# Kernel tuning notes

Hardware: AMD Instinct MI355X
Metric: run time of the kernel (lower is better)

The kernel has to match this reference:

```python
import jax, jax.numpy as jnp
import numpy as np

IMAGE_SIZE = (128, 128)
NUM_SLICES = 4
SLICE_SPACING = 0.1
BACKGROUND = 0.0
CHUNK = 1024
N_GAUSS = 4096
EPS = 1e-6


def setup_inputs() -> dict:
    key = jax.random.key(0)
    k1, k2, k3, k4, k5 = jax.random.split(key, 5)
    return {
        "means": jax.random.uniform(k1, (N_GAUSS, 3), dtype=jnp.float32),
        "scales": jax.random.uniform(k2, (N_GAUSS, 3), dtype=jnp.float32),
        "rotations": jax.random.normal(k3, (N_GAUSS, 4), dtype=jnp.float32),
        "opacities": jax.random.uniform(k4, (N_GAUSS, 1), dtype=jnp.float32),
        "features": jax.random.uniform(k5, (N_GAUSS, 1), dtype=jnp.float32),
    }


def _quat_to_rot(q):
    # q: [N,4] (w,x,y,z) -> [N,3,3]
    q = q / jnp.linalg.norm(q, axis=1, keepdims=True)
    w, x, y, z = q[:, 0], q[:, 1], q[:, 2], q[:, 3]
    r0 = jnp.stack([1 - 2 * (y * y + z * z), 2 * (x * y - w * z), 2 * (x * z + w * y)], axis=-1)
    r1 = jnp.stack([2 * (x * y + w * z), 1 - 2 * (x * x + z * z), 2 * (y * z - w * x)], axis=-1)
    r2 = jnp.stack([2 * (x * z - w * y), 2 * (y * z + w * x), 1 - 2 * (x * x + y * y)], axis=-1)
    return jnp.stack([r0, r1, r2], axis=-2)


def _forward(means, scales, rotations, opacities, features):
    H, W = IMAGE_SIZE
    dtype = means.dtype
    P = H * W

    # 3D covariance: Sigma = (R S)(R S)^T
    R = _quat_to_rot(rotations)
    RS = R * scales[:, None, :]
    cov = RS @ jnp.swapaxes(RS, 1, 2)  # [N,3,3]

    # slice z positions and shared pixel grid
    total_depth = (NUM_SLICES - 1) * SLICE_SPACING
    zs = jnp.linspace(-total_depth / 2, total_depth / 2, NUM_SLICES)
    yy, xx = jnp.meshgrid(jnp.linspace(-1, 1, H), jnp.linspace(-1, 1, W), indexing="ij")
    grid = jnp.stack([xx, yy], axis=-1).reshape(P, 2).astype(dtype)

    # conditional (marginal-at-z) 2D covariance, slice independent
    sxy = cov[:, :2, :2]                     # [N,2,2]
    sxz = cov[:, :2, 2]                      # [N,2]
    szz = cov[:, 2, 2]                       # [N]
    sigma2d = sxy - (sxz[:, :, None] * sxz[:, None, :]) / (szz + EPS)[:, None, None]
    sigma2d = sigma2d + EPS * jnp.eye(2, dtype=dtype)
    a, b = sigma2d[:, 0, 0], sigma2d[:, 0, 1]
    c, d = sigma2d[:, 1, 0], sigma2d[:, 1, 1]
    det = a * d - b * c
    inv2d = jnp.stack([jnp.stack([d, -b], -1), jnp.stack([-c, a], -1)], -2) / det[:, None, None]

    max_dist = 3.0 * scales[:, 2].max()

    nch = N_GAUSS // CHUNK
    rs = lambda t: t.reshape((nch, CHUNK) + t.shape[1:])
    chunks = (rs(means), rs(inv2d), rs(sxz), rs(szz), rs(opacities[:, 0]), rs(features[:, 0]))

    def render_slice(slice_z):
        def body(carry, ch):
            img, acc = carry
            mu, invk, sxzk, szzk, op, ft = ch
            mask = (jnp.abs(mu[:, 2] - slice_z) < max_dist).astype(dtype)  # all-pass by construction
            zoff = slice_z - mu[:, 2]
            mu2d = mu[:, :2] + sxzk / (szzk + EPS)[:, None] * zoff[:, None]  # [K,2]
            off = grid[:, None, :] - mu2d[None, :, :]                        # [P,K,2]
            maha = jnp.einsum("pki,kij,pkj->pk", off, invk, off)
            g = jnp.exp(-0.5 * maha) * mask[None, :]                         # [P,K]
            weight = (1 - acc)[:, None] * (g * op[None, :])
            img = img + (weight * (g * ft[None, :])).sum(-1)
            acc = acc + weight.sum(-1)
            return (img, acc), None

        init = (jnp.zeros(P, dtype), jnp.zeros(P, dtype))
        (img, acc), _ = jax.lax.scan(body, init, chunks)
        img = img + (1 - acc) * BACKGROUND
        return img.reshape(H, W)

    return jnp.stack([render_slice(zs[s]) for s in range(NUM_SLICES)], axis=0)


def reference(means, scales, rotations, opacities, features):
    return _forward(means, scales, rotations, opacities, features)
```

## Files before the change

kernel.cpp:

```cpp
#include <hip/hip_runtime.h>


#define EPSV 1e-6f
#define NG   4096
#define PP   16384
#define NSL  4
#define GSEG 128
#define SUBB 16

__global__ void prep_kernel(const float* __restrict__ means,
                            const float* __restrict__ scales,
                            const float* __restrict__ rots,
                            const float* __restrict__ ops,
                            const float* __restrict__ fts,
                            float4* __restrict__ gdata) {
    __shared__ float red[256];
    int tid = threadIdx.x;

    float m = -1e30f;
    for (int i = tid; i < NG; i += 256) m = fmaxf(m, scales[i*3+2]);
    red[tid] = m;
    __syncthreads();
    for (int s = 128; s > 0; s >>= 1) {
        if (tid < s) red[tid] = fmaxf(red[tid], red[tid+s]);
        __syncthreads();
    }
    float maxd = 3.0f * red[0];

    int g = blockIdx.x * 256 + tid;
    if (g >= NG) return;

    float qw = rots[g*4+0], qx = rots[g*4+1], qy = rots[g*4+2], qz = rots[g*4+3];
    float inorm = rsqrtf(qw*qw + qx*qx + qy*qy + qz*qz);
    qw *= inorm; qx *= inorm; qy *= inorm; qz *= inorm;

    float s0 = scales[g*3+0], s1 = scales[g*3+1], s2 = scales[g*3+2];

    float r00 = 1.f - 2.f*(qy*qy + qz*qz), r01 = 2.f*(qx*qy - qw*qz), r02 = 2.f*(qx*qz + qw*qy);
    float r10 = 2.f*(qx*qy + qw*qz), r11 = 1.f - 2.f*(qx*qx + qz*qz), r12 = 2.f*(qy*qz - qw*qx);
    float r20 = 2.f*(qx*qz - qw*qy), r21 = 2.f*(qy*qz + qw*qx), r22 = 1.f - 2.f*(qx*qx + qy*qy);

    float a00 = r00*s0, a01 = r01*s1, a02 = r02*s2;
    float a10 = r10*s0, a11 = r11*s1, a12 = r12*s2;
    float a20 = r20*s0, a21 = r21*s1, a22 = r22*s2;

    float c00 = a00*a00 + a01*a01 + a02*a02;
    float c01 = a00*a10 + a01*a11 + a02*a12;
    float c02 = a00*a20 + a01*a21 + a02*a22;
    float c11 = a10*a10 + a11*a11 + a12*a12;
    float c12 = a10*a20 + a11*a21 + a12*a22;
    float c22 = a20*a20 + a21*a21 + a22*a22;

    float izz = 1.0f / (c22 + EPSV);
    float kx = c02 * izz, ky = c12 * izz;
    float sa = c00 - c02*c02*izz + EPSV;
    float sb = c01 - c02*c12*izz;
    float sd = c11 - c12*c12*izz + EPSV;
    float det = sa*sd - sb*sb;
    float idet = 1.0f / det;

    const float C0 = -0.72134752044448170f;
    float qa = C0 * sd * idet;
    float qb = C0 * (-2.0f * sb * idet);
    float qd = C0 * sa * idet;

    float mx = means[g*3+0], my = means[g*3+1], mz = means[g*3+2];
    float op = ops[g], ft = fts[g];

    #pragma unroll
    for (int s = 0; s < NSL; ++s) {
        float z = -0.15f + 0.1f * (float)s;
        float zoff = z - mz;
        float m2x = mx + kx * zoff;
        float m2y = my + ky * zoff;
        bool live = (fabsf(mz - z) < maxd) && (op > 1e-12f);
        float lop  = live ? __log2f(op) : -__builtin_inff();
        float ftop = live ? ft / op     : 0.f;
        float c3 = -(2.0f*qa*m2x + qb*m2y);
        float c4 = -(2.0f*qd*m2y + qb*m2x);
        float c5 = qa*m2x*m2x + qb*m2x*m2y + qd*m2y*m2y + lop;
        float4* o = gdata + ((size_t)(s*NG + g)) * 2;
        o[0] = make_float4(qa, qb, qd, c3);
        o[1] = make_float4(c4, c5, ftop, 0.f);
    }
}

__global__ __launch_bounds__(512, 4)
void render_kernel(const float4* __restrict__ gdata, float2* __restrict__ part) {
    int tid   = threadIdx.x;
    int lane  = tid & 63;
    int w     = __builtin_amdgcn_readfirstlane(tid >> 6);
    int b     = blockIdx.x;
    int cs    = b & 31;
    int band  = b >> 5;
    int slice = band >> 2;
    int ch    = w & 1;
    int rbase = (band & 3) * 32 + (w >> 1) * 8;

    const float DL = 2.0f / 127.0f;
    float x = -1.0f + (float)(ch * 64 + lane) * DL;

    float yv[8];
    #pragma unroll
    for (int j = 0; j < 8; ++j) yv[j] = -1.0f + (float)(rbase + j) * DL;

    const float4* base = gdata + ((size_t)slice * NG + cs * GSEG) * 2;

    float s1[8], s2[8];
    #pragma unroll
    for (int j = 0; j < 8; ++j) { s1[j] = 0.f; s2[j] = 0.f; }

    for (int kk = 0; kk < 8; ++kk) {
        int sb = (w + kk) & 7;
        const float4* q = base + sb * SUBB * 2;
        #pragma unroll 8
        for (int t = 0; t < SUBB; ++t) {
            float4 A = q[2*t+0];
            float4 B = q[2*t+1];
            float A1 = fmaf(A.x, x, A.w);
            float A2 = fmaf(A.y, x, B.x);
            float A3 = fmaf(A1,  x, B.y);
            #pragma unroll
            for (int j = 0; j < 8; ++j) {
                float wj = fmaf(A.z, yv[j], A2);
                float mj = fmaf(wj, yv[j], A3);
                float gj = __builtin_amdgcn_exp2f(mj);
                s1[j] += gj;
                s2[j] = fmaf(gj * gj, B.z, s2[j]);
            }
        }
    }

    size_t ob = (size_t)cs * (NSL * PP) + (size_t)slice * PP
              + (size_t)rbase * 128 + ch * 64 + lane;
    #pragma unroll
    for (int j = 0; j < 8; ++j)
        part[ob + (size_t)j * 128] = make_float2(s1[j], s2[j]);
}

__global__ __launch_bounds__(256)
void combine_kernel(const float2* __restrict__ part, float* __restrict__ out) {
    int px = blockIdx.x * 256 + threadIdx.x;
    float img = 0.f, acc = 0.f;
    #pragma unroll
    for (int c = 0; c < 4; ++c) {
        float S1 = 0.f, S2 = 0.f;
        #pragma unroll
        for (int s = 0; s < 8; ++s) {
            float2 v = part[(size_t)(c*8 + s) * (NSL*PP) + px];
            S1 += v.x;  S2 += v.y;
        }
        float om = 1.0f - acc;
        img = fmaf(om, S2, img);
        acc = fmaf(om, S1, acc);
    }
    out[px] = img;
}

extern "C" void kernel_launch(void* const* d_in, const int* in_sizes, int n_in,
                              void* d_out, int out_size, void* d_ws, size_t ws_size,
                              hipStream_t stream) {
    const float* means  = (const float*)d_in[0];
    const float* scales = (const float*)d_in[1];
    const float* rots   = (const float*)d_in[2];
    const float* ops    = (const float*)d_in[3];
    const float* fts    = (const float*)d_in[4];
    float* out = (float*)d_out;

    float4* gdata = (float4*)d_ws;
    float2* part  = (float2*)((char*)d_ws + (size_t)NSL*NG*32);

    prep_kernel<<<NG/256, 256, 0, stream>>>(means, scales, rots, ops, fts, gdata);
    render_kernel<<<512, 512, 0, stream>>>(gdata, part);
    combine_kernel<<<NSL*PP/256, 256, 0, stream>>>(part, out);
}
```

Before: 121.0 us.

## Split render work into more, smaller blocks with finer gaussian segments

Shrinks render blocks from 512 to 256 threads covering 16 rows instead of 32. Gaussian chunks are split into 16 segments of 64 (or 8 of 128 if workspace is small), which raises the grid to 2048 blocks for better occupancy and load balance. The cost is more partial-sum buffers, so combine reads twice as many partials and moves more memory. The path is chosen by workspace size at runtime.

```diff
diff --git a/kernel.cpp b/kernel.cpp
--- a/kernel.cpp
+++ b/kernel.cpp
@@ -5,8 +5,9 @@
 #define NG   4096
 #define PP   16384
 #define NSL  4
-#define GSEG 128
 #define SUBB 16
+
+typedef float v2f __attribute__((ext_vector_type(2)));
 
 __global__ void prep_kernel(const float* __restrict__ means,
                             const float* __restrict__ scales,
@@ -85,17 +86,22 @@
     }
 }
 
-__global__ __launch_bounds__(512, 4)
+template<int NSEG>
+__global__ __launch_bounds__(256, 8)
 void render_kernel(const float4* __restrict__ gdata, float2* __restrict__ part) {
+    constexpr int GSEGT = 1024 / NSEG;
+    constexpr int NSB   = GSEGT / SUBB;
+    constexpr int NCS   = 4 * NSEG;
+
     int tid   = threadIdx.x;
     int lane  = tid & 63;
     int w     = __builtin_amdgcn_readfirstlane(tid >> 6);
     int b     = blockIdx.x;
-    int cs    = b & 31;
-    int band  = b >> 5;
-    int slice = band >> 2;
+    int cs    = b & (NCS - 1);
+    int band  = b / NCS;
+    int slice = band >> 3;
     int ch    = w & 1;
-    int rbase = (band & 3) * 32 + (w >> 1) * 8;
+    int rbase = (band & 7) * 16 + (w >> 1) * 8;
 
     const float DL = 2.0f / 127.0f;
     float x = -1.0f + (float)(ch * 64 + lane) * DL;
@@ -104,14 +110,14 @@
     #pragma unroll
     for (int j = 0; j < 8; ++j) yv[j] = -1.0f + (float)(rbase + j) * DL;
 
-    const float4* base = gdata + ((size_t)slice * NG + cs * GSEG) * 2;
+    const float4* base = gdata + ((size_t)slice * NG + cs * GSEGT) * 2;
 
     float s1[8], s2[8];
     #pragma unroll
     for (int j = 0; j < 8; ++j) { s1[j] = 0.f; s2[j] = 0.f; }
 
-    for (int kk = 0; kk < 8; ++kk) {
-        int sb = (w + kk) & 7;
+    for (int kk = 0; kk < NSB; ++kk) {
+        int sb = (w + kk) & (NSB - 1);
         const float4* q = base + sb * SUBB * 2;
         #pragma unroll 8
         for (int t = 0; t < SUBB; ++t) {
@@ -138,6 +144,7 @@
         part[ob + (size_t)j * 128] = make_float2(s1[j], s2[j]);
 }
 
+template<int NSEG>
 __global__ __launch_bounds__(256)
 void combine_kernel(const float2* __restrict__ part, float* __restrict__ out) {
     int px = blockIdx.x * 256 + threadIdx.x;
@@ -146,8 +153,8 @@
     for (int c = 0; c < 4; ++c) {
         float S1 = 0.f, S2 = 0.f;
         #pragma unroll
-        for (int s = 0; s < 8; ++s) {
-            float2 v = part[(size_t)(c*8 + s) * (NSL*PP) + px];
+        for (int s = 0; s < NSEG; ++s) {
+            float2 v = part[(size_t)(c*NSEG + s) * (NSL*PP) + px];
             S1 += v.x;  S2 += v.y;
         }
         float om = 1.0f - acc;
@@ -171,6 +178,13 @@
     float2* part  = (float2*)((char*)d_ws + (size_t)NSL*NG*32);
 
     prep_kernel<<<NG/256, 256, 0, stream>>>(means, scales, rots, ops, fts, gdata);
-    render_kernel<<<512, 512, 0, stream>>>(gdata, part);
-    combine_kernel<<<NSL*PP/256, 256, 0, stream>>>(part, out);
+
+    size_t need16 = (size_t)NSL*NG*32 + (size_t)64 * (NSL*PP) * sizeof(float2);
+    if (ws_size >= need16) {
+        render_kernel<16><<<64 * 32, 256, 0, stream>>>(gdata, part);
+        combine_kernel<16><<<NSL*PP/256, 256, 0, stream>>>(part, out);
+    } else {
+        render_kernel<8><<<32 * 32, 256, 0, stream>>>(gdata, part);
+        combine_kernel<8><<<NSL*PP/256, 256, 0, stream>>>(part, out);
+    }
 }
```

New measurement: 129.6 us. 7.1% more time.

## Broadcast gaussian params via readlane and rescale exp to drop a multiply

Applied to the files above, without the earlier changes.

The gaussian parameters move to two split float4 arrays. Each wave loads 128 gaussians once into registers, one per lane, and broadcasts them with readlane, so the inner loop no longer issues repeated uniform global loads. The prep kernel folds a sqrt(feature/opacity) factor into the exponent offset. The inner loop can then use h*rr and h*h fmas instead of a separate square and multiply. Blocks shrink to 256 threads with 1024 blocks, which raises occupancy but adds readlane SALU/VALU traffic and an fmax clamp that can perturb numerics for tiny features.

```diff
diff --git a/kernel.cpp b/kernel.cpp
--- a/kernel.cpp
+++ b/kernel.cpp
@@ -5,15 +5,18 @@
 #define NG   4096
 #define PP   16384
 #define NSL  4
+#define NCS  32
 #define GSEG 128
-#define SUBB 16
+
+#define RL(v, g) __int_as_float(__builtin_amdgcn_readlane(__float_as_int(v), (g)))
 
 __global__ void prep_kernel(const float* __restrict__ means,
                             const float* __restrict__ scales,
                             const float* __restrict__ rots,
                             const float* __restrict__ ops,
                             const float* __restrict__ fts,
-                            float4* __restrict__ gdata) {
+                            float4* __restrict__ gA,
+                            float4* __restrict__ gB) {
     __shared__ float red[256];
     int tid = threadIdx.x;
 
@@ -74,28 +77,41 @@
         float m2x = mx + kx * zoff;
         float m2y = my + ky * zoff;
         bool live = (fabsf(mz - z) < maxd) && (op > 1e-12f);
-        float lop  = live ? __log2f(op) : -__builtin_inff();
-        float ftop = live ? ft / op     : 0.f;
+
         float c3 = -(2.0f*qa*m2x + qb*m2y);
         float c4 = -(2.0f*qd*m2y + qb*m2x);
-        float c5 = qa*m2x*m2x + qb*m2x*m2y + qd*m2y*m2y + lop;
-        float4* o = gdata + ((size_t)(s*NG + g)) * 2;
-        o[0] = make_float4(qa, qb, qd, c3);
-        o[1] = make_float4(c4, c5, ftop, 0.f);
-    }
-}
-
-__global__ __launch_bounds__(512, 4)
-void render_kernel(const float4* __restrict__ gdata, float2* __restrict__ part) {
+        float c5q = qa*m2x*m2x + qb*m2x*m2y + qd*m2y*m2y;
+
+        float c5p, rr;
+        if (live) {
+            float lop  = __log2f(op);
+            float ftop = fmaxf(ft / op, 1e-20f);
+            float L    = 0.5f * __log2f(ftop);
+            c5p = c5q + lop + L;
+            rr  = exp2f(-L);
+        } else {
+            c5p = -__builtin_inff();
+            rr  = 0.f;
+        }
+        size_t o = (size_t)s * NG + g;
+        gA[o] = make_float4(qa, qb, qd, c3);
+        gB[o] = make_float4(c4, c5p, rr, 0.f);
+    }
+}
+
+__global__ __launch_bounds__(256, 6)
+void render_kernel(const float4* __restrict__ gA,
+                   const float4* __restrict__ gB,
+                   float2* __restrict__ part) {
     int tid   = threadIdx.x;
     int lane  = tid & 63;
     int w     = __builtin_amdgcn_readfirstlane(tid >> 6);
     int b     = blockIdx.x;
-    int cs    = b & 31;
+    int cs    = b & (NCS - 1);
     int band  = b >> 5;
-    int slice = band >> 2;
+    int slice = band >> 3;
     int ch    = w & 1;
-    int rbase = (band & 3) * 32 + (w >> 1) * 8;
+    int rbase = (band & 7) * 16 + (w >> 1) * 8;
 
     const float DL = 2.0f / 127.0f;
     float x = -1.0f + (float)(ch * 64 + lane) * DL;
@@ -104,29 +120,36 @@
     #pragma unroll
     for (int j = 0; j < 8; ++j) yv[j] = -1.0f + (float)(rbase + j) * DL;
 
-    const float4* base = gdata + ((size_t)slice * NG + cs * GSEG) * 2;
-
     float s1[8], s2[8];
     #pragma unroll
     for (int j = 0; j < 8; ++j) { s1[j] = 0.f; s2[j] = 0.f; }
 
-    for (int kk = 0; kk < 8; ++kk) {
-        int sb = (w + kk) & 7;
-        const float4* q = base + sb * SUBB * 2;
+    size_t segoff = (size_t)slice * NG + (size_t)cs * GSEG;
+    float4 vA0 = gA[segoff + lane];
+    float4 vB0 = gB[segoff + lane];
+    float4 vA1 = gA[segoff + 64 + lane];
+    float4 vB1 = gB[segoff + 64 + lane];
+
+    #pragma unroll 1
+    for (int batch = 0; batch < 2; ++batch) {
+        float4 vA = batch ? vA1 : vA0;
+        float4 vB = batch ? vB1 : vB0;
         #pragma unroll 8
-        for (int t = 0; t < SUBB; ++t) {
-            float4 A = q[2*t+0];
-            float4 B = q[2*t+1];
-            float A1 = fmaf(A.x, x, A.w);
-            float A2 = fmaf(A.y, x, B.x);
-            float A3 = fmaf(A1,  x, B.y);
+        for (int g = 0; g < 64; ++g) {
+            float c0 = RL(vA.x, g), c1 = RL(vA.y, g);
+            float c2 = RL(vA.z, g), c3 = RL(vA.w, g);
+            float c4 = RL(vB.x, g), c5 = RL(vB.y, g);
+            float rr = RL(vB.z, g);
+            float A1 = fmaf(c0, x, c3);
+            float A2 = fmaf(c1, x, c4);
+            float A3 = fmaf(A1, x, c5);
             #pragma unroll
             for (int j = 0; j < 8; ++j) {
-                float wj = fmaf(A.z, yv[j], A2);
+                float wj = fmaf(c2, yv[j], A2);
                 float mj = fmaf(wj, yv[j], A3);
-                float gj = __builtin_amdgcn_exp2f(mj);
-                s1[j] += gj;
-                s2[j] = fmaf(gj * gj, B.z, s2[j]);
+                float h  = __builtin_amdgcn_exp2f(mj);
+                s1[j] = fmaf(h, rr, s1[j]);
+                s2[j] = fmaf(h, h,  s2[j]);
             }
         }
     }
@@ -167,10 +190,11 @@
     const float* fts    = (const float*)d_in[4];
     float* out = (float*)d_out;
 
-    float4* gdata = (float4*)d_ws;
-    float2* part  = (float2*)((char*)d_ws + (size_t)NSL*NG*32);
-
-    prep_kernel<<<NG/256, 256, 0, stream>>>(means, scales, rots, ops, fts, gdata);
-    render_kernel<<<512, 512, 0, stream>>>(gdata, part);
+    float4* gA   = (float4*)d_ws;
+    float4* gB   = (float4*)((char*)d_ws + (size_t)NSL*NG*16);
+    float2* part = (float2*)((char*)d_ws + (size_t)NSL*NG*32);
+
+    prep_kernel<<<NG/256, 256, 0, stream>>>(means, scales, rots, ops, fts, gA, gB);
+    render_kernel<<<NCS * 32, 256, 0, stream>>>(gA, gB, part);
     combine_kernel<<<NSL*PP/256, 256, 0, stream>>>(part, out);
 }
```

Result: slower. 137.2 us (+13.4%).

## Fold feature ratio into exponent, stage gaussians in LDS, halve block size

Applied to the files above, without the earlier changes.

The prep kernel now folds half of log2(ft/op) into the exponent constant and stores its inverse as a per-gaussian factor. The inner render loop then computes h*h and h*rr with plain FMAs, removing the separate g*g multiply. The render kernel stages each block's 128 gaussians in shared memory once, instead of every wave reading them from global memory. Blocks are now 256 threads over 16 rows with twice as many blocks, which raises parallelism. The trade is a clamp on ft/op at 1e-20, which can change results when features are near zero.

```diff
diff --git a/kernel.cpp b/kernel.cpp
--- a/kernel.cpp
+++ b/kernel.cpp
@@ -5,8 +5,8 @@
 #define NG   4096
 #define PP   16384
 #define NSL  4
+#define NCS  32
 #define GSEG 128
-#define SUBB 16
 
 __global__ void prep_kernel(const float* __restrict__ means,
                             const float* __restrict__ scales,
@@ -74,28 +74,44 @@
         float m2x = mx + kx * zoff;
         float m2y = my + ky * zoff;
         bool live = (fabsf(mz - z) < maxd) && (op > 1e-12f);
-        float lop  = live ? __log2f(op) : -__builtin_inff();
-        float ftop = live ? ft / op     : 0.f;
+
         float c3 = -(2.0f*qa*m2x + qb*m2y);
         float c4 = -(2.0f*qd*m2y + qb*m2x);
-        float c5 = qa*m2x*m2x + qb*m2x*m2y + qd*m2y*m2y + lop;
-        float4* o = gdata + ((size_t)(s*NG + g)) * 2;
+        float c5q = qa*m2x*m2x + qb*m2x*m2y + qd*m2y*m2y;
+
+        float c5p, rr;
+        if (live) {
+            float lop  = __log2f(op);
+            float ftop = fmaxf(ft / op, 1e-20f);
+            float L    = 0.5f * __log2f(ftop);
+            c5p = c5q + lop + L;
+            rr  = exp2f(-L);
+        } else {
+            c5p = -__builtin_inff();
+            rr  = 0.f;
+        }
+        float4* o = gdata + ((size_t)s * NG + g) * 2;
         o[0] = make_float4(qa, qb, qd, c3);
-        o[1] = make_float4(c4, c5, ftop, 0.f);
+        o[1] = make_float4(c4, c5p, rr, 0.f);
     }
 }
 
-__global__ __launch_bounds__(512, 4)
+__global__ __launch_bounds__(256, 4)
 void render_kernel(const float4* __restrict__ gdata, float2* __restrict__ part) {
+    __shared__ float4 sg[GSEG * 2];
+
     int tid   = threadIdx.x;
     int lane  = tid & 63;
     int w     = __builtin_amdgcn_readfirstlane(tid >> 6);
     int b     = blockIdx.x;
-    int cs    = b & 31;
+    int cs    = b & (NCS - 1);
     int band  = b >> 5;
-    int slice = band >> 2;
+    int slice = band >> 3;
     int ch    = w & 1;
-    int rbase = (band & 3) * 32 + (w >> 1) * 8;
+    int rbase = (band & 7) * 16 + (w >> 1) * 8;
+
+    sg[tid] = gdata[((size_t)slice * NG + (size_t)cs * GSEG) * 2 + tid];
+    __syncthreads();
 
     const float DL = 2.0f / 127.0f;
     float x = -1.0f + (float)(ch * 64 + lane) * DL;
@@ -104,30 +120,25 @@
     #pragma unroll
     for (int j = 0; j < 8; ++j) yv[j] = -1.0f + (float)(rbase + j) * DL;
 
-    const float4* base = gdata + ((size_t)slice * NG + cs * GSEG) * 2;
-
     float s1[8], s2[8];
     #pragma unroll
     for (int j = 0; j < 8; ++j) { s1[j] = 0.f; s2[j] = 0.f; }
 
-    for (int kk = 0; kk < 8; ++kk) {
-        int sb = (w + kk) & 7;
-        const float4* q = base + sb * SUBB * 2;
-        #pragma unroll 8
-        for (int t = 0; t < SUBB; ++t) {
-            float4 A = q[2*t+0];
-            float4 B = q[2*t+1];
-            float A1 = fmaf(A.x, x, A.w);
-            float A2 = fmaf(A.y, x, B.x);
-            float A3 = fmaf(A1,  x, B.y);
-            #pragma unroll
-            for (int j = 0; j < 8; ++j) {
-                float wj = fmaf(A.z, yv[j], A2);
-                float mj = fmaf(wj, yv[j], A3);
-                float gj = __builtin_amdgcn_exp2f(mj);
-                s1[j] += gj;
-                s2[j] = fmaf(gj * gj, B.z, s2[j]);
-            }
+    #pragma unroll 4
+    for (int g = 0; g < GSEG; ++g) {
+        float4 A = sg[2*g+0];
+        float4 B = sg[2*g+1];
+        float A1 = fmaf(A.x, x, A.w);
+        float A2 = fmaf(A.y, x, B.x);
+        float A3 = fmaf(A1,  x, B.y);
+        float rr = B.z;
+        #pragma unroll
+        for (int j = 0; j < 8; ++j) {
+            float wj = fmaf(A.z, yv[j], A2);
+            float mj = fmaf(wj, yv[j], A3);
+            float h  = __builtin_amdgcn_exp2f(mj);
+            s1[j] = fmaf(h, rr, s1[j]);
+            s2[j] = fmaf(h, h,  s2[j]);
         }
     }
 
@@ -171,6 +182,6 @@
     float2* part  = (float2*)((char*)d_ws + (size_t)NSL*NG*32);
 
     prep_kernel<<<NG/256, 256, 0, stream>>>(means, scales, rots, ops, fts, gdata);
-    render_kernel<<<512, 512, 0, stream>>>(gdata, part);
+    render_kernel<<<NCS * 32, 256, 0, stream>>>(gdata, part);
     combine_kernel<<<NSL*PP/256, 256, 0, stream>>>(part, out);
 }
```

Measured after the change: 128.3 us. 6.0% more time.
